# Kernel optimization log

Measured on AMD Instinct MI355X. Metric: run time of the kernel, lower is better.

Reference implementation:

```python
import jax, jax.numpy as jnp
import numpy as np

V, D, NH, DH, DFF, NL = 32000, 512, 8, 64, 2048, 6
S, B = 512, 8
NEG = -1e18


def layer_norm(x, g, b, eps=1e-5):
    m = x.mean(-1, keepdims=True)
    v = ((x - m) ** 2).mean(-1, keepdims=True)
    return (x - m) / jnp.sqrt(v + eps) * g + b


def mha(q, k, v, Wq, bq, Wk, bk, Wv, bv, Wo, bo, mask):
    Bq, Q, _ = q.shape
    K = k.shape[1]
    qh = (q @ Wq + bq).reshape(Bq, Q, NH, DH).transpose(0, 2, 1, 3)
    kh = (k @ Wk + bk).reshape(Bq, K, NH, DH).transpose(0, 2, 1, 3)
    vh = (v @ Wv + bv).reshape(Bq, K, NH, DH).transpose(0, 2, 1, 3)
    scores = jnp.einsum('bhqd,bhkd->bhqk', qh, kh) / np.sqrt(DH).astype(np.float32)
    scores = jnp.where(mask[:, None, :, :], NEG, scores)
    attn = jax.nn.softmax(scores, axis=-1)
    ctx = jnp.einsum('bhqk,bhkd->bhqd', attn, vh).transpose(0, 2, 1, 3).reshape(Bq, Q, NH * DH)
    return ctx @ Wo + bo


def positional_encoding(seq_len):
    pos = jnp.arange(seq_len, dtype=jnp.float32)[:, None]
    div = jnp.exp(jnp.arange(0, D, 2, dtype=jnp.float32) * (-np.log(10000.0) / D))
    pe = jnp.zeros((seq_len, D), jnp.float32)
    pe = pe.at[:, 0::2].set(jnp.sin(pos * div))
    pe = pe.at[:, 1::2].set(jnp.cos(pos * div))
    return pe


def setup_inputs() -> dict:
    key = jax.random.key(0)
    ks = iter(jax.random.split(key, 64))
    sc = 0.02
    pn = lambda shape: jax.random.normal(next(ks), shape, jnp.float32) * sc
    inp = {}
    inp['targets'] = jax.random.randint(next(ks), (S, B), 0, V)
    inp['memory'] = jax.random.normal(next(ks), (B, S, D), jnp.float32)
    inp['trg_mask'] = jnp.broadcast_to(jnp.triu(jnp.ones((S, S), bool), 1), (B, S, S))
    inp['memory_mask'] = jnp.zeros((B, S, S), bool)
    emb = pn((V, D)).at[1].set(0.0)  # padding_idx=1
    inp['emb'] = emb
    # stacked per-layer params
    for nm in ['Wq_s', 'Wk_s', 'Wv_s', 'Wo_s', 'Wq_c', 'Wk_c', 'Wv_c', 'Wo_c']:
        inp[nm] = pn((NL, D, D))
    for nm in ['bq_s', 'bk_s', 'bv_s', 'bo_s', 'bq_c', 'bk_c', 'bv_c', 'bo_c']:
        inp[nm] = jnp.zeros((NL, D), jnp.float32)
    inp['W1'] = pn((NL, D, DFF)); inp['b1'] = jnp.zeros((NL, DFF), jnp.float32)
    inp['W2'] = pn((NL, DFF, D)); inp['b2'] = jnp.zeros((NL, D), jnp.float32)
    for nm in ['g1', 'g2', 'g3']:
        inp[nm] = jnp.ones((NL, D), jnp.float32)
    for nm in ['be1', 'be2', 'be3']:
        inp[nm] = jnp.zeros((NL, D), jnp.float32)
    return inp


def reference(targets, memory, trg_mask, memory_mask, emb,
              Wq_s, bq_s, Wk_s, bk_s, Wv_s, bv_s, Wo_s, bo_s,
              Wq_c, bq_c, Wk_c, bk_c, Wv_c, bv_c, Wo_c, bo_c,
              W1, b1, W2, b2, g1, be1, g2, be2, g3, be3):
    # targets: (S, B) ints; embedding + sqrt(d) scale + sinusoidal PE
    x = emb[targets] * np.sqrt(D).astype(np.float32)      # (S, B, D)
    x = x + positional_encoding(targets.shape[0])[:, None, :]
    x = x.transpose(1, 0, 2)                              # (B, S, D)
    for i in range(NL):
        sa = mha(x, x, x, Wq_s[i], bq_s[i], Wk_s[i], bk_s[i], Wv_s[i], bv_s[i],
                 Wo_s[i], bo_s[i], trg_mask)
        x = layer_norm(x + sa, g1[i], be1[i])
        ca = mha(x, memory, memory, Wq_c[i], bq_c[i], Wk_c[i], bk_c[i], Wv_c[i], bv_c[i],
                 Wo_c[i], bo_c[i], memory_mask)
        x = layer_norm(x + ca, g2[i], be2[i])
        ff = jax.nn.relu(x @ W1[i] + b1[i]) @ W2[i] + b2[i]
        x = layer_norm(x + ff, g3[i], be3[i])
    return x
```

## Files before the change

### kernel.cpp

```cpp
#include <hip/hip_runtime.h>

typedef unsigned short u16;
typedef unsigned int   u32;
typedef __attribute__((ext_vector_type(4))) u16   u16x4;
typedef __attribute__((ext_vector_type(8))) u16   u16x8;
typedef __attribute__((ext_vector_type(8))) __bf16 bf16x8;
typedef __attribute__((ext_vector_type(4))) float f32x4;

#define DEV static __device__ __forceinline__

constexpr int DIM = 512, NHEAD = 8, DHEAD = 64, DFFN = 2048, NLAY = 6, SEQ = 512, BATCH = 8;
constexpr int MROWS = BATCH * SEQ;
constexpr long HD = (long)SEQ * DHEAD;
constexpr long SQ = (long)DIM * DIM;

DEV float bf2f(u16 u) { union { u32 i; float f; } x; x.i = (u32)u << 16; return x.f; }
DEV u16 f2bf(float f) { union { float f; u32 i; } x; x.f = f; u32 r = x.i + 0x7fffu + ((x.i >> 16) & 1u); return (u16)(r >> 16); }

DEV void gl_lds16(const u16* g, u16* l) {
    __builtin_amdgcn_global_load_lds((const __attribute__((address_space(1))) u32*)(const void*)g,
                                     (__attribute__((address_space(3))) u32*)(void*)l, 16, 0, 0);
}

struct TP { const float* in[8]; u16* out[8]; long ls[8]; };

__global__ __launch_bounds__(256) void transpose8(TP p)
{
    __shared__ u16 t[32][33];
    int z = blockIdx.z, which = z / NLAY, l = z % NLAY;
    const float* in = p.in[which] + (long)l * SQ;
    u16* out = p.out[which] + (long)l * p.ls[which];
    int k0 = blockIdx.y * 32, n0 = blockIdx.x * 32;
    int tx = threadIdx.x & 31, ty = threadIdx.x >> 5;
    #pragma unroll
    for (int i = ty; i < 32; i += 8) t[i][tx] = f2bf(in[(long)(k0 + i) * 512 + n0 + tx]);
    __syncthreads();
    #pragma unroll
    for (int i = ty; i < 32; i += 8) out[(long)(n0 + i) * 512 + k0 + tx] = t[tx][i];
}

__global__ __launch_bounds__(256) void transpose_w(const float* __restrict__ in, u16* __restrict__ out,
                                                   int K, int N, long outLS)
{
    __shared__ u16 t[32][33];
    long bi = (long)blockIdx.z * K * N, bo = (long)blockIdx.z * outLS;
    int k0 = blockIdx.y * 32, n0 = blockIdx.x * 32;
    int tx = threadIdx.x & 31, ty = threadIdx.x >> 5;
    #pragma unroll
    for (int i = ty; i < 32; i += 8) t[i][tx] = f2bf(in[bi + (long)(k0 + i) * N + n0 + tx]);
    __syncthreads();
    #pragma unroll
    for (int i = ty; i < 32; i += 8) out[bo + (long)(n0 + i) * K + k0 + tx] = t[tx][i];
}

__global__ __launch_bounds__(256) void concat_bias(const float* __restrict__ a, const float* __restrict__ b,
                                                   const float* __restrict__ c, float* __restrict__ out, int nsrc)
{
    int i = blockIdx.x * 256 + threadIdx.x;
    int col = i & 511, j = (i >> 9) % nsrc, l = i / (nsrc * 512);
    const float* s = (j == 0) ? a : (j == 1) ? b : c;
    out[i] = s[l * 512 + col];
}

__global__ __launch_bounds__(256) void conv_f32_bf16(const float* __restrict__ in, u16* __restrict__ out)
{
    long i = ((long)blockIdx.x * 256 + threadIdx.x) * 4;
    float4 v = *(const float4*)(in + i);
    u16x4 o; o.x = f2bf(v.x); o.y = f2bf(v.y); o.z = f2bf(v.z); o.w = f2bf(v.w);
    *(u16x4*)(out + i) = o;
}

__global__ __launch_bounds__(256) void embed_pe(const int* __restrict__ targets, const float* __restrict__ emb,
                                                u16* __restrict__ xb)
{
    int t4 = (blockIdx.x * 256 + threadIdx.x) * 4;
    int d = t4 & (DIM - 1);
    int s = (t4 >> 9) & (SEQ - 1);
    int b = t4 >> 18;
    int tok = targets[s * BATCH + b];
    float4 e = *(const float4*)(emb + (long)tok * DIM + d);
    u16x4 ob;
    const float ef[4] = { e.x, e.y, e.z, e.w };
    #pragma unroll
    for (int j = 0; j < 4; ++j) {
        int dd = d + j;
        float div = expf((float)(dd & ~1) * -0.017988946039016f);
        float ang = (float)s * div;
        float pe = (dd & 1) ? cosf(ang) : sinf(ang);
        ob[j] = f2bf(ef[j] * 22.627416997969522f + pe);
    }
    *(u16x4*)(xb + ((long)b * SEQ + s) * DIM + d) = ob;
}

DEV void scat_sd(u16* dst, int mm, int col, float v) {
    dst[(long)((mm >> 9) * NHEAD + (col >> 6)) * HD + (long)(mm & 511) * DHEAD + (col & 63)] = f2bf(v);
}
DEV void scat_ds(u16* dst, int mm, int col, float v) {
    dst[(long)((mm >> 9) * NHEAD + (col >> 6)) * HD + (long)(col & 63) * SEQ + (mm & 511)] = f2bf(v);
}

template <int BM, int BN, int EPI>
__global__ __launch_bounds__(256) void gemm_t(const u16* __restrict__ A0, const u16* __restrict__ A1,
                                              const u16* __restrict__ Bt,
                                              void* __restrict__ C0, void* __restrict__ C1, void* __restrict__ C2,
                                              const float* __restrict__ bias, int K, int ld, int ldc,
                                              int gx, int aSplit)
{
    constexpr int NCHA = BM / 8;
    constexpr int NCH  = (BM + BN) / 8;
    constexpr int MI   = BM / 32;
    constexpr int NI   = BN / 32;
    __shared__ __align__(16) u16 lds[2][NCH * 512];

    const int tid = threadIdx.x, lane = tid & 63, wid = tid >> 6;
    const int nwg = gridDim.x, bid = blockIdx.x;
    const int wg = (bid & 7) * (nwg >> 3) + (bid >> 3);
    const int m0 = (wg / gx) * BM, n0 = (wg % gx) * BN;
    const u16* A = (n0 < aSplit) ? A0 : A1;
    const int kBase = blockIdx.y * K;
    const int wr = (wid >> 1) * (BM / 2), wc = (wid & 1) * (BN / 2);
    const int fr = lane & 15, fq = lane >> 4;
    const int srow = lane >> 3;
    const int scol = ((lane & 7) ^ srow) * 8;

    f32x4 acc[MI][NI] = {};

    auto stage = [&](int buf, int k0) {
        #pragma unroll
        for (int c = wid; c < NCH; c += 4) {
            if (c < NCHA) gl_lds16(A  + (long)(m0 + c * 8 + srow) * ld + kBase + k0 + scol, &lds[buf][c * 512]);
            else          gl_lds16(Bt + (long)(n0 + (c - NCHA) * 8 + srow) * ld + kBase + k0 + scol, &lds[buf][c * 512]);
        }
    };

    const int nt = K >> 6;
    stage(0, 0);
    __syncthreads();
    int cur = 0;
    const int swz = (fr & 7) << 4;
    for (int t = 0; t < nt; ++t) {
        if (t + 1 < nt) stage(cur ^ 1, (t + 1) << 6);
        const char* lb = (const char*)&lds[cur][0];
        bf16x8 a[MI][2], b[NI][2];
        #pragma unroll
        for (int mi = 0; mi < MI; ++mi)
            #pragma unroll
            for (int kk = 0; kk < 2; ++kk)
                a[mi][kk] = *(const bf16x8*)(lb + (wr + mi * 16 + fr) * 128 + ((kk * 64 + fq * 16) ^ swz));
        #pragma unroll
        for (int ni = 0; ni < NI; ++ni)
            #pragma unroll
            for (int kk = 0; kk < 2; ++kk)
                b[ni][kk] = *(const bf16x8*)(lb + (BM + wc + ni * 16 + fr) * 128 + ((kk * 64 + fq * 16) ^ swz));
        #pragma unroll
        for (int kk = 0; kk < 2; ++kk)
            #pragma unroll
            for (int mi = 0; mi < MI; ++mi)
                #pragma unroll
                for (int ni = 0; ni < NI; ++ni)
                    acc[mi][ni] = __builtin_amdgcn_mfma_f32_16x16x32_bf16(a[mi][kk], b[ni][kk], acc[mi][ni], 0, 0, 0);
        __syncthreads();
        cur ^= 1;
    }

    #pragma unroll
    for (int mi = 0; mi < MI; ++mi)
    #pragma unroll
    for (int ni = 0; ni < NI; ++ni)
    #pragma unroll
    for (int rr = 0; rr < 4; ++rr) {
        int mm = m0 + wr + mi * 16 + fq * 4 + rr;
        int nn = n0 + wc + ni * 16 + fr;
        float v = acc[mi][ni][rr];
        if (EPI != 5) v += bias[nn];
        if (EPI == 0) {
            ((u16*)C0)[(long)mm * ldc + nn] = f2bf(v);
        } else if (EPI == 1) {
            ((u16*)C0)[(long)mm * ldc + nn] = f2bf(fmaxf(v, 0.f));
        } else if (EPI == 5) {
            ((float*)C0)[(long)blockIdx.y * MROWS * ldc + (long)mm * ldc + nn] = v;
        } else {
            int which = nn >> 9, col = nn & 511;
            if (which == 0)      scat_sd((u16*)C0, mm, col, v);
            else if (which == 1) scat_sd((u16*)C1, mm, col, v);
            else                 scat_ds((u16*)C2, mm, col, v);
        }
    }
}

template <bool CAUSAL>
__global__ __launch_bounds__(256) void flash_attn(const u16* __restrict__ qh, const u16* __restrict__ kh,
                                                  const u16* __restrict__ vT, u16* __restrict__ ctx)
{
    constexpr int KVB = 128;
    __shared__ __align__(16) u16 Kl[2][KVB * 64];
    __shared__ __align__(16) u16 Vl[2][64 * KVB];
    __shared__ __align__(16) u16 Pl[4][16 * KVB];
    const int lane = threadIdx.x & 63, wid = threadIdx.x >> 6;
    const int head = blockIdx.x & 63, qt = blockIdx.x >> 6;
    const int q0 = qt * 64;
    const long hb = (long)head * HD;
    const int fr = lane & 15, fq = lane >> 4;
    const int swz = (fr & 7) << 4;

    bf16x8 qf[2];
    #pragma unroll
    for (int kf = 0; kf < 2; ++kf)
        qf[kf] = *(const bf16x8*)(qh + hb + (long)(q0 + wid * 16 + fr) * 64 + kf * 32 + fq * 8);

    const int nt = CAUSAL ? (q0 >> 7) + 1 : SEQ / KVB;

    auto stage = [&](int buf, int t) {
        const long kv0 = (long)t * KVB;
        const int kr = lane >> 3;
        const int kcol = ((lane & 7) ^ kr) * 8;
        for (int c = wid; c < 16; c += 4)
            gl_lds16(kh + hb + (kv0 + c * 8 + kr) * 64 + kcol, &Kl[buf][c * 512]);
        const int vr = lane >> 4;
        for (int c = wid; c < 16; c += 4) {
            int row = c * 4 + vr;
            int vcol = ((lane & 15) ^ (row & 7)) * 8;
            gl_lds16(vT + hb + (long)row * SEQ + kv0 + vcol, &Vl[buf][c * 512]);
        }
    };

    float m[4], l[4];
    #pragma unroll
    for (int r = 0; r < 4; ++r) { m[r] = -3.0e38f; l[r] = 0.f; }
    f32x4 ao[4] = {};

    stage(0, 0);
    __syncthreads();
    int cur = 0;
    for (int t = 0; t < nt; ++t) {
        if (t + 1 < nt) stage(cur ^ 1, t + 1);
        f32x4 as[8] = {};
        const char* kb = (const char*)&Kl[cur][0];
        __builtin_amdgcn_s_setprio(1);
        #pragma unroll
        for (int nf = 0; nf < 8; ++nf)
            #pragma unroll
            for (int kf = 0; kf < 2; ++kf) {
                bf16x8 kfr = *(const bf16x8*)(kb + (nf * 16 + fr) * 128 + ((kf * 64 + fq * 16) ^ swz));
                as[nf] = __builtin_amdgcn_mfma_f32_16x16x32_bf16(qf[kf], kfr, as[nf], 0, 0, 0);
            }
        __builtin_amdgcn_s_setprio(0);
        const int kv0 = t * KVB;
        const int qrow = q0 + wid * 16 + fq * 4;
        #pragma unroll
        for (int nf = 0; nf < 8; ++nf)
            #pragma unroll
            for (int rr = 0; rr < 4; ++rr) {
                float s = as[nf][rr] * 0.125f;
                if (CAUSAL && (kv0 + nf * 16 + fr > qrow + rr)) s = -3.0e38f;
                as[nf][rr] = s;
            }
        float p_scale[4];
        #pragma unroll
        for (int rr = 0; rr < 4; ++rr) {
            float mx = as[0][rr];
            #pragma unroll
            for (int nf = 1; nf < 8; ++nf) mx = fmaxf(mx, as[nf][rr]);
            #pragma unroll
            for (int o = 1; o < 16; o <<= 1) mx = fmaxf(mx, __shfl_xor(mx, o, 64));
            float mnew = fmaxf(m[rr], mx);
            p_scale[rr] = __expf(m[rr] - mnew);
            m[rr] = mnew;
        }
        float rsum[4] = {0.f, 0.f, 0.f, 0.f};
        u16* pw = &Pl[wid][0];
        #pragma unroll
        for (int nf = 0; nf < 8; ++nf)
            #pragma unroll
            for (int rr = 0; rr < 4; ++rr) {
                float p = __expf(as[nf][rr] - m[rr]);
                rsum[rr] += p;
                int row = fq * 4 + rr;
                int byte = (row * 256 + (nf * 16 + fr) * 2) ^ ((row & 7) << 4);
                *(u16*)((char*)pw + byte) = f2bf(p);
            }
        #pragma unroll
        for (int rr = 0; rr < 4; ++rr) {
            #pragma unroll
            for (int o = 1; o < 16; o <<= 1) rsum[rr] += __shfl_xor(rsum[rr], o, 64);
            l[rr] = l[rr] * p_scale[rr] + rsum[rr];
        }
        #pragma unroll
        for (int nf = 0; nf < 4; ++nf)
            #pragma unroll
            for (int rr = 0; rr < 4; ++rr) ao[nf][rr] *= p_scale[rr];
        const char* vb = (const char*)&Vl[cur][0];
        __builtin_amdgcn_s_setprio(1);
        #pragma unroll
        for (int kf = 0; kf < 4; ++kf) {
            int pbyte = (fr * 256 + kf * 64 + fq * 16) ^ swz;
            bf16x8 pa = *(const bf16x8*)((const char*)pw + pbyte);
            #pragma unroll
            for (int nf = 0; nf < 4; ++nf) {
                bf16x8 vf = *(const bf16x8*)(vb + (nf * 16 + fr) * 256 + ((kf * 64 + fq * 16) ^ swz));
                ao[nf] = __builtin_amdgcn_mfma_f32_16x16x32_bf16(pa, vf, ao[nf], 0, 0, 0);
            }
        }
        __builtin_amdgcn_s_setprio(0);
        __syncthreads();
        cur ^= 1;
    }
    const int b = head >> 3, h = head & 7;
    #pragma unroll
    for (int nf = 0; nf < 4; ++nf)
        #pragma unroll
        for (int rr = 0; rr < 4; ++rr) {
            int qq = q0 + wid * 16 + fq * 4 + rr;
            ctx[((long)(b * SEQ + qq)) * DIM + h * 64 + nf * 16 + fr] = f2bf(ao[nf][rr] / l[rr]);
        }
}

__global__ __launch_bounds__(256) void add_ln(u16* xb, const u16* __restrict__ y,
                                              const float* __restrict__ g, const float* __restrict__ be)
{
    int row = blockIdx.x * 4 + (threadIdx.x >> 6);
    int lane = threadIdx.x & 63;
    long off = (long)row * DIM + lane * 8;
    u16x8 xv = *(const u16x8*)(xb + off);
    u16x8 yv = *(const u16x8*)(y + off);
    float v[8];
    #pragma unroll
    for (int j = 0; j < 8; ++j) v[j] = bf2f(xv[j]) + bf2f(yv[j]);
    float sum = 0.f;
    #pragma unroll
    for (int j = 0; j < 8; ++j) sum += v[j];
    #pragma unroll
    for (int o = 32; o; o >>= 1) sum += __shfl_xor(sum, o, 64);
    float mean = sum * (1.0f / DIM);
    float vs = 0.f;
    #pragma unroll
    for (int j = 0; j < 8; ++j) { float d = v[j] - mean; vs += d * d; }
    #pragma unroll
    for (int o = 32; o; o >>= 1) vs += __shfl_xor(vs, o, 64);
    float rstd = rsqrtf(vs * (1.0f / DIM) + 1e-5f);
    u16x8 ob;
    #pragma unroll
    for (int j = 0; j < 8; ++j) {
        int col = lane * 8 + j;
        ob[j] = f2bf((v[j] - mean) * rstd * g[col] + be[col]);
    }
    *(u16x8*)(xb + off) = ob;
}

__global__ __launch_bounds__(256) void add_ln2(u16* xb, const float* __restrict__ yf,
                                               const float* __restrict__ bias,
                                               const float* __restrict__ g, const float* __restrict__ be,
                                               float* __restrict__ xf)
{
    int row = blockIdx.x * 4 + (threadIdx.x >> 6);
    int lane = threadIdx.x & 63;
    long off = (long)row * DIM + lane * 8;
    u16x8 xv = *(const u16x8*)(xb + off);
    float4 a0 = *(const float4*)(yf + off);
    float4 a1 = *(const float4*)(yf + off + 4);
    float4 b0 = *(const float4*)(yf + (long)MROWS * DIM + off);
    float4 b1 = *(const float4*)(yf + (long)MROWS * DIM + off + 4);
    float v[8] = { a0.x + b0.x, a0.y + b0.y, a0.z + b0.z, a0.w + b0.w,
                   a1.x + b1.x, a1.y + b1.y, a1.z + b1.z, a1.w + b1.w };
    #pragma unroll
    for (int j = 0; j < 8; ++j) v[j] += bf2f(xv[j]) + bias[lane * 8 + j];
    float sum = 0.f;
    #pragma unroll
    for (int j = 0; j < 8; ++j) sum += v[j];
    #pragma unroll
    for (int o = 32; o; o >>= 1) sum += __shfl_xor(sum, o, 64);
    float mean = sum * (1.0f / DIM);
    float vs = 0.f;
    #pragma unroll
    for (int j = 0; j < 8; ++j) { float d = v[j] - mean; vs += d * d; }
    #pragma unroll
    for (int o = 32; o; o >>= 1) vs += __shfl_xor(vs, o, 64);
    float rstd = rsqrtf(vs * (1.0f / DIM) + 1e-5f);
    float outv[8]; u16x8 ob;
    #pragma unroll
    for (int j = 0; j < 8; ++j) {
        int col = lane * 8 + j;
        float r = (v[j] - mean) * rstd * g[col] + be[col];
        outv[j] = r; ob[j] = f2bf(r);
    }
    *(u16x8*)(xb + off) = ob;
    if (xf) {
        *(float4*)(xf + off)     = *(const float4*)&outv[0];
        *(float4*)(xf + off + 4) = *(const float4*)&outv[4];
    }
}

extern "C" void kernel_launch(void* const* d_in, const int* in_sizes, int n_in,
                              void* d_out, int out_size, void* d_ws, size_t ws_size,
                              hipStream_t stream)
{
    const int*   targets = (const int*)  d_in[0];
    const float* memory  = (const float*)d_in[1];
    const float* emb     = (const float*)d_in[4];
    const float* Wg[8]; for (int i = 0; i < 8; ++i) Wg[i] = (const float*)d_in[5 + i];
    const float* bg[8]; for (int i = 0; i < 8; ++i) bg[i] = (const float*)d_in[13 + i];
    const float* W1  = (const float*)d_in[21];
    const float* b1  = (const float*)d_in[22];
    const float* W2  = (const float*)d_in[23];
    const float* b2  = (const float*)d_in[24];
    const float* g1  = (const float*)d_in[25];
    const float* g2  = (const float*)d_in[26];
    const float* g3  = (const float*)d_in[27];
    const float* be1 = (const float*)d_in[28];
    const float* be2 = (const float*)d_in[29];
    const float* be3 = (const float*)d_in[30];

    char* w = (char*)d_ws;
    auto take = [&](size_t n) -> char* { char* p = w; w += (n + 255) & ~(size_t)255; return p; };
    u16*   wqkvT = (u16*)take((size_t)NLAY * 3 * SQ * 2);
    u16*   wcatT = (u16*)take((size_t)NLAY * 3 * SQ * 2);
    u16*   woT   = (u16*)take((size_t)NLAY * SQ * 2);
    u16*   wocT  = (u16*)take((size_t)NLAY * SQ * 2);
    u16*   w1T   = (u16*)take((size_t)NLAY * DIM * DFFN * 2);
    u16*   w2T   = (u16*)take((size_t)NLAY * DIM * DFFN * 2);
    float* bqkv  = (float*)take((size_t)NLAY * 3 * DIM * 4);
    float* bqkvc = (float*)take((size_t)NLAY * 3 * DIM * 4);
    u16*   xb    = (u16*)  take((size_t)MROWS * DIM * 2);
    u16*   y     = (u16*)  take((size_t)MROWS * DIM * 2);
    float* yf    = (float*)take((size_t)2 * MROWS * DIM * 4);
    u16*   memb  = (u16*)  take((size_t)MROWS * DIM * 2);
    u16*   qh    = (u16*)  take((size_t)MROWS * DIM * 2);
    u16*   kh    = (u16*)  take((size_t)MROWS * DIM * 2);
    u16*   vT    = (u16*)  take((size_t)MROWS * DIM * 2);
    u16*   ctx   = (u16*)  take((size_t)MROWS * DIM * 2);
    u16*   h1    = (u16*)  take((size_t)MROWS * DFFN * 2);

    TP tp;
    tp.in[0] = Wg[0]; tp.out[0] = wqkvT;          tp.ls[0] = 3 * SQ;
    tp.in[1] = Wg[1]; tp.out[1] = wqkvT + SQ;     tp.ls[1] = 3 * SQ;
    tp.in[2] = Wg[2]; tp.out[2] = wqkvT + 2 * SQ; tp.ls[2] = 3 * SQ;
    tp.in[3] = Wg[3]; tp.out[3] = woT;            tp.ls[3] = SQ;
    tp.in[4] = Wg[4]; tp.out[4] = wcatT;          tp.ls[4] = 3 * SQ;
    tp.in[5] = Wg[5]; tp.out[5] = wcatT + SQ;     tp.ls[5] = 3 * SQ;
    tp.in[6] = Wg[6]; tp.out[6] = wcatT + 2 * SQ; tp.ls[6] = 3 * SQ;
    tp.in[7] = Wg[7]; tp.out[7] = wocT;           tp.ls[7] = SQ;
    transpose8<<<dim3(16, 16, 8 * NLAY), 256, 0, stream>>>(tp);
    transpose_w<<<dim3(64, 16, NLAY), 256, 0, stream>>>(W1, w1T, DIM, DFFN, (long)DIM * DFFN);
    transpose_w<<<dim3(16, 64, NLAY), 256, 0, stream>>>(W2, w2T, DFFN, DIM, (long)DIM * DFFN);
    concat_bias<<<NLAY * 3 * DIM / 256, 256, 0, stream>>>(bg[0], bg[1], bg[2], bqkv, 3);
    concat_bias<<<NLAY * 3 * DIM / 256, 256, 0, stream>>>(bg[4], bg[5], bg[6], bqkvc, 3);
    conv_f32_bf16<<<2048, 256, 0, stream>>>(memory, memb);
    embed_pe<<<2048, 256, 0, stream>>>(targets, emb, xb);

    const int BIG = 1 << 30;
    for (int i = 0; i < NLAY; ++i) {
        const u16 *wqkv = wqkvT + (long)i * 3 * SQ, *wcat = wcatT + (long)i * 3 * SQ;
        const u16 *wo = woT + (long)i * SQ, *woc = wocT + (long)i * SQ;
        const u16 *w1t = w1T + (long)i * DIM * DFFN, *w2t = w2T + (long)i * DIM * DFFN;
        const float *bo = bg[3] + i * DIM, *boc = bg[7] + i * DIM;

        gemm_t<128, 128, 4><<<384, 256, 0, stream>>>(xb, xb, wqkv, qh, kh, vT, bqkv + i * 3 * DIM, DIM, DIM, 0, 12, BIG);
        flash_attn<true><<<BATCH * NHEAD * (SEQ / 64), 256, 0, stream>>>(qh, kh, vT, ctx);
        gemm_t<64, 64, 0><<<512, 256, 0, stream>>>(ctx, ctx, wo, y, nullptr, nullptr, bo, DIM, DIM, DIM, 8, BIG);
        add_ln<<<MROWS / 4, 256, 0, stream>>>(xb, y, g1 + i * DIM, be1 + i * DIM);

        gemm_t<128, 128, 4><<<384, 256, 0, stream>>>(xb, memb, wcat, qh, kh, vT, bqkvc + i * 3 * DIM, DIM, DIM, 0, 12, 512);
        flash_attn<false><<<BATCH * NHEAD * (SEQ / 64), 256, 0, stream>>>(qh, kh, vT, ctx);
        gemm_t<64, 64, 0><<<512, 256, 0, stream>>>(ctx, ctx, woc, y, nullptr, nullptr, boc, DIM, DIM, DIM, 8, BIG);
        add_ln<<<MROWS / 4, 256, 0, stream>>>(xb, y, g2 + i * DIM, be2 + i * DIM);

        gemm_t<128, 128, 1><<<512, 256, 0, stream>>>(xb, xb, w1t, h1, nullptr, nullptr, b1 + i * DFFN, DIM, DIM, DFFN, 16, BIG);
        gemm_t<64, 64, 5><<<dim3(512, 2), 256, 0, stream>>>(h1, h1, w2t, yf, nullptr, nullptr, nullptr,
                                                            DFFN / 2, DFFN, DIM, 8, BIG);
        add_ln2<<<MROWS / 4, 256, 0, stream>>>(xb, yf, b2 + i * DIM, g3 + i * DIM, be3 + i * DIM,
                                               (i == NLAY - 1) ? (float*)d_out : nullptr);
    }
}
```

Before: 817.9 us.

## Merge prep kernels, add BK template for small GEMMs, lazy softmax rescale

The GEMM is templated on its K tile. The 64x64 GEMMs (output projections and FFN2) now use a K tile of 128, which halves their loop iterations and barriers, and the swizzle is generalised to match. Flash attention now rescales the running max and accumulators only when some row's max grows by more than 8, skipping exponentials and multiplies on most tiles at some cost to numeric headroom. Several setup kernels are merged into fewer launches (W1/W2 transposes, the bias concats, and embedding plus memory conversion) to cut launch overhead.

```diff
diff --git a/kernel.cpp b/kernel.cpp
--- a/kernel.cpp
+++ b/kernel.cpp
@@ -39,57 +39,66 @@
     for (int i = ty; i < 32; i += 8) out[(long)(n0 + i) * 512 + k0 + tx] = t[tx][i];
 }
 
-__global__ __launch_bounds__(256) void transpose_w(const float* __restrict__ in, u16* __restrict__ out,
-                                                   int K, int N, long outLS)
+__global__ __launch_bounds__(256) void transpose_w12(const float* __restrict__ W1, const float* __restrict__ W2,
+                                                     u16* __restrict__ w1T, u16* __restrict__ w2T)
 {
     __shared__ u16 t[32][33];
-    long bi = (long)blockIdx.z * K * N, bo = (long)blockIdx.z * outLS;
-    int k0 = blockIdx.y * 32, n0 = blockIdx.x * 32;
+    int z = blockIdx.z;
+    bool isW2 = z >= NLAY;
+    int l = isW2 ? z - NLAY : z;
+    const float* in = (isW2 ? W2 : W1) + (long)l * DIM * DFFN;
+    u16* out = (isW2 ? w2T : w1T) + (long)l * DIM * DFFN;
+    int K = isW2 ? DFFN : DIM, N = isW2 ? DIM : DFFN;
+    int k0 = (isW2 ? blockIdx.x : blockIdx.y) * 32;
+    int n0 = (isW2 ? blockIdx.y : blockIdx.x) * 32;
     int tx = threadIdx.x & 31, ty = threadIdx.x >> 5;
     #pragma unroll
-    for (int i = ty; i < 32; i += 8) t[i][tx] = f2bf(in[bi + (long)(k0 + i) * N + n0 + tx]);
+    for (int i = ty; i < 32; i += 8) t[i][tx] = f2bf(in[(long)(k0 + i) * N + n0 + tx]);
     __syncthreads();
     #pragma unroll
-    for (int i = ty; i < 32; i += 8) out[bo + (long)(n0 + i) * K + k0 + tx] = t[tx][i];
-}
-
-__global__ __launch_bounds__(256) void concat_bias(const float* __restrict__ a, const float* __restrict__ b,
-                                                   const float* __restrict__ c, float* __restrict__ out, int nsrc)
+    for (int i = ty; i < 32; i += 8) out[(long)(n0 + i) * K + k0 + tx] = t[tx][i];
+}
+
+struct CB { const float* s[6]; };
+__global__ __launch_bounds__(256) void concat2(CB p, float* __restrict__ bqkv, float* __restrict__ bqkvc)
 {
     int i = blockIdx.x * 256 + threadIdx.x;
-    int col = i & 511, j = (i >> 9) % nsrc, l = i / (nsrc * 512);
-    const float* s = (j == 0) ? a : (j == 1) ? b : c;
-    out[i] = s[l * 512 + col];
-}
-
-__global__ __launch_bounds__(256) void conv_f32_bf16(const float* __restrict__ in, u16* __restrict__ out)
-{
-    long i = ((long)blockIdx.x * 256 + threadIdx.x) * 4;
-    float4 v = *(const float4*)(in + i);
-    u16x4 o; o.x = f2bf(v.x); o.y = f2bf(v.y); o.z = f2bf(v.z); o.w = f2bf(v.w);
-    *(u16x4*)(out + i) = o;
-}
-
-__global__ __launch_bounds__(256) void embed_pe(const int* __restrict__ targets, const float* __restrict__ emb,
-                                                u16* __restrict__ xb)
-{
-    int t4 = (blockIdx.x * 256 + threadIdx.x) * 4;
-    int d = t4 & (DIM - 1);
-    int s = (t4 >> 9) & (SEQ - 1);
-    int b = t4 >> 18;
-    int tok = targets[s * BATCH + b];
-    float4 e = *(const float4*)(emb + (long)tok * DIM + d);
-    u16x4 ob;
-    const float ef[4] = { e.x, e.y, e.z, e.w };
-    #pragma unroll
-    for (int j = 0; j < 4; ++j) {
-        int dd = d + j;
-        float div = expf((float)(dd & ~1) * -0.017988946039016f);
-        float ang = (float)s * div;
-        float pe = (dd & 1) ? cosf(ang) : sinf(ang);
-        ob[j] = f2bf(ef[j] * 22.627416997969522f + pe);
-    }
-    *(u16x4*)(xb + ((long)b * SEQ + s) * DIM + d) = ob;
+    constexpr int HALF = NLAY * 3 * DIM;
+    int j = (i < HALF) ? i : i - HALF;
+    int col = j & 511, wsel = (j >> 9) % 3, l = j / 1536;
+    const float* s = p.s[(i < HALF ? 0 : 3) + wsel];
+    (i < HALF ? bqkv : bqkvc)[j] = s[l * 512 + col];
+}
+
+__global__ __launch_bounds__(256) void prep_act(const int* __restrict__ targets, const float* __restrict__ emb,
+                                                u16* __restrict__ xb,
+                                                const float* __restrict__ memory, u16* __restrict__ memb)
+{
+    int bid = blockIdx.x;
+    if (bid < 2048) {
+        int t4 = (bid * 256 + threadIdx.x) * 4;
+        int d = t4 & (DIM - 1);
+        int s = (t4 >> 9) & (SEQ - 1);
+        int b = t4 >> 18;
+        int tok = targets[s * BATCH + b];
+        float4 e = *(const float4*)(emb + (long)tok * DIM + d);
+        u16x4 ob;
+        const float ef[4] = { e.x, e.y, e.z, e.w };
+        #pragma unroll
+        for (int j = 0; j < 4; ++j) {
+            int dd = d + j;
+            float div = expf((float)(dd & ~1) * -0.017988946039016f);
+            float ang = (float)s * div;
+            float pe = (dd & 1) ? cosf(ang) : sinf(ang);
+            ob[j] = f2bf(ef[j] * 22.627416997969522f + pe);
+        }
+        *(u16x4*)(xb + ((long)b * SEQ + s) * DIM + d) = ob;
+    } else {
+        long i = ((long)(bid - 2048) * 256 + threadIdx.x) * 4;
+        float4 v = *(const float4*)(memory + i);
+        u16x4 o; o.x = f2bf(v.x); o.y = f2bf(v.y); o.z = f2bf(v.z); o.w = f2bf(v.w);
+        *(u16x4*)(memb + i) = o;
+    }
 }
 
 DEV void scat_sd(u16* dst, int mm, int col, float v) {
@@ -99,17 +108,20 @@
     dst[(long)((mm >> 9) * NHEAD + (col >> 6)) * HD + (long)(col & 63) * SEQ + (mm & 511)] = f2bf(v);
 }
 
-template <int BM, int BN, int EPI>
+template <int BM, int BN, int BK, int EPI>
 __global__ __launch_bounds__(256) void gemm_t(const u16* __restrict__ A0, const u16* __restrict__ A1,
                                               const u16* __restrict__ Bt,
                                               void* __restrict__ C0, void* __restrict__ C1, void* __restrict__ C2,
                                               const float* __restrict__ bias, int K, int ld, int ldc,
                                               int gx, int aSplit)
 {
-    constexpr int NCHA = BM / 8;
-    constexpr int NCH  = (BM + BN) / 8;
-    constexpr int MI   = BM / 32;
-    constexpr int NI   = BN / 32;
+    constexpr int SLOTS = BK / 8;
+    constexpr int RPC   = 512 / BK;
+    constexpr int KK    = BK / 32;
+    constexpr int NCHA  = BM / RPC;
+    constexpr int NCH   = (BM + BN) / RPC;
+    constexpr int MI    = BM / 32;
+    constexpr int NI    = BN / 32;
     __shared__ __align__(16) u16 lds[2][NCH * 512];
 
     const int tid = threadIdx.x, lane = tid & 63, wid = tid >> 6;
@@ -120,40 +132,43 @@
     const int kBase = blockIdx.y * K;
     const int wr = (wid >> 1) * (BM / 2), wc = (wid & 1) * (BN / 2);
     const int fr = lane & 15, fq = lane >> 4;
-    const int srow = lane >> 3;
-    const int scol = ((lane & 7) ^ srow) * 8;
+    const int srow  = lane / SLOTS;
+    const int sslot = lane % SLOTS;
 
     f32x4 acc[MI][NI] = {};
 
     auto stage = [&](int buf, int k0) {
         #pragma unroll
         for (int c = wid; c < NCH; c += 4) {
-            if (c < NCHA) gl_lds16(A  + (long)(m0 + c * 8 + srow) * ld + kBase + k0 + scol, &lds[buf][c * 512]);
-            else          gl_lds16(Bt + (long)(n0 + (c - NCHA) * 8 + srow) * ld + kBase + k0 + scol, &lds[buf][c * 512]);
+            int slot = sslot ^ ((c * RPC + srow) & (SLOTS - 1));
+            long row = (c < NCHA) ? (long)(m0 + c * RPC + srow)
+                                  : (long)(n0 + (c - NCHA) * RPC + srow);
+            const u16* src = (c < NCHA) ? A : Bt;
+            gl_lds16(src + row * ld + kBase + k0 + slot * 8, &lds[buf][c * 512]);
         }
     };
 
-    const int nt = K >> 6;
+    const int nt = K / BK;
     stage(0, 0);
     __syncthreads();
     int cur = 0;
-    const int swz = (fr & 7) << 4;
+    const int swz = (fr & (SLOTS - 1)) << 4;
     for (int t = 0; t < nt; ++t) {
-        if (t + 1 < nt) stage(cur ^ 1, (t + 1) << 6);
+        if (t + 1 < nt) stage(cur ^ 1, (t + 1) * BK);
         const char* lb = (const char*)&lds[cur][0];
-        bf16x8 a[MI][2], b[NI][2];
+        bf16x8 a[MI][KK], b[NI][KK];
         #pragma unroll
         for (int mi = 0; mi < MI; ++mi)
             #pragma unroll
-            for (int kk = 0; kk < 2; ++kk)
-                a[mi][kk] = *(const bf16x8*)(lb + (wr + mi * 16 + fr) * 128 + ((kk * 64 + fq * 16) ^ swz));
+            for (int kk = 0; kk < KK; ++kk)
+                a[mi][kk] = *(const bf16x8*)(lb + (wr + mi * 16 + fr) * (BK * 2) + ((kk * 64 + fq * 16) ^ swz));
         #pragma unroll
         for (int ni = 0; ni < NI; ++ni)
             #pragma unroll
-            for (int kk = 0; kk < 2; ++kk)
-                b[ni][kk] = *(const bf16x8*)(lb + (BM + wc + ni * 16 + fr) * 128 + ((kk * 64 + fq * 16) ^ swz));
-        #pragma unroll
-        for (int kk = 0; kk < 2; ++kk)
+            for (int kk = 0; kk < KK; ++kk)
+                b[ni][kk] = *(const bf16x8*)(lb + (BM + wc + ni * 16 + fr) * (BK * 2) + ((kk * 64 + fq * 16) ^ swz));
+        #pragma unroll
+        for (int kk = 0; kk < KK; ++kk)
             #pragma unroll
             for (int mi = 0; mi < MI; ++mi)
                 #pragma unroll
@@ -255,7 +270,7 @@
                 if (CAUSAL && (kv0 + nf * 16 + fr > qrow + rr)) s = -3.0e38f;
                 as[nf][rr] = s;
             }
-        float p_scale[4];
+        float mnew[4]; int need = 0;
         #pragma unroll
         for (int rr = 0; rr < 4; ++rr) {
             float mx = as[0][rr];
@@ -263,9 +278,18 @@
             for (int nf = 1; nf < 8; ++nf) mx = fmaxf(mx, as[nf][rr]);
             #pragma unroll
             for (int o = 1; o < 16; o <<= 1) mx = fmaxf(mx, __shfl_xor(mx, o, 64));
-            float mnew = fmaxf(m[rr], mx);
-            p_scale[rr] = __expf(m[rr] - mnew);
-            m[rr] = mnew;
+            mnew[rr] = fmaxf(m[rr], mx);
+            need |= (mx > m[rr] + 8.f) ? 1 : 0;
+        }
+        if (__any(need)) {
+            #pragma unroll
+            for (int rr = 0; rr < 4; ++rr) {
+                float ps = __expf(m[rr] - mnew[rr]);
+                m[rr] = mnew[rr];
+                l[rr] *= ps;
+                #pragma unroll
+                for (int nf = 0; nf < 4; ++nf) ao[nf][rr] *= ps;
+            }
         }
         float rsum[4] = {0.f, 0.f, 0.f, 0.f};
         u16* pw = &Pl[wid][0];
@@ -283,12 +307,8 @@
         for (int rr = 0; rr < 4; ++rr) {
             #pragma unroll
             for (int o = 1; o < 16; o <<= 1) rsum[rr] += __shfl_xor(rsum[rr], o, 64);
-            l[rr] = l[rr] * p_scale[rr] + rsum[rr];
-        }
-        #pragma unroll
-        for (int nf = 0; nf < 4; ++nf)
-            #pragma unroll
-            for (int rr = 0; rr < 4; ++rr) ao[nf][rr] *= p_scale[rr];
+            l[rr] += rsum[rr];
+        }
         const char* vb = (const char*)&Vl[cur][0];
         __builtin_amdgcn_s_setprio(1);
         #pragma unroll
@@ -440,12 +460,11 @@
     tp.in[6] = Wg[6]; tp.out[6] = wcatT + 2 * SQ; tp.ls[6] = 3 * SQ;
     tp.in[7] = Wg[7]; tp.out[7] = wocT;           tp.ls[7] = SQ;
     transpose8<<<dim3(16, 16, 8 * NLAY), 256, 0, stream>>>(tp);
-    transpose_w<<<dim3(64, 16, NLAY), 256, 0, stream>>>(W1, w1T, DIM, DFFN, (long)DIM * DFFN);
-    transpose_w<<<dim3(16, 64, NLAY), 256, 0, stream>>>(W2, w2T, DFFN, DIM, (long)DIM * DFFN);
-    concat_bias<<<NLAY * 3 * DIM / 256, 256, 0, stream>>>(bg[0], bg[1], bg[2], bqkv, 3);
-    concat_bias<<<NLAY * 3 * DIM / 256, 256, 0, stream>>>(bg[4], bg[5], bg[6], bqkvc, 3);
-    conv_f32_bf16<<<2048, 256, 0, stream>>>(memory, memb);
-    embed_pe<<<2048, 256, 0, stream>>>(targets, emb, xb);
+    transpose_w12<<<dim3(64, 16, 2 * NLAY), 256, 0, stream>>>(W1, W2, w1T, w2T);
+    CB cb; cb.s[0] = bg[0]; cb.s[1] = bg[1]; cb.s[2] = bg[2];
+    cb.s[3] = bg[4]; cb.s[4] = bg[5]; cb.s[5] = bg[6];
+    concat2<<<2 * NLAY * 3 * DIM / 256, 256, 0, stream>>>(cb, bqkv, bqkvc);
+    prep_act<<<4096, 256, 0, stream>>>(targets, emb, xb, memory, memb);
 
     const int BIG = 1 << 30;
     for (int i = 0; i < NLAY; ++i) {
@@ -454,19 +473,19 @@
         const u16 *w1t = w1T + (long)i * DIM * DFFN, *w2t = w2T + (long)i * DIM * DFFN;
         const float *bo = bg[3] + i * DIM, *boc = bg[7] + i * DIM;
 
-        gemm_t<128, 128, 4><<<384, 256, 0, stream>>>(xb, xb, wqkv, qh, kh, vT, bqkv + i * 3 * DIM, DIM, DIM, 0, 12, BIG);
+        gemm_t<128, 128, 64, 4><<<384, 256, 0, stream>>>(xb, xb, wqkv, qh, kh, vT, bqkv + i * 3 * DIM, DIM, DIM, 0, 12, BIG);
         flash_attn<true><<<BATCH * NHEAD * (SEQ / 64), 256, 0, stream>>>(qh, kh, vT, ctx);
-        gemm_t<64, 64, 0><<<512, 256, 0, stream>>>(ctx, ctx, wo, y, nullptr, nullptr, bo, DIM, DIM, DIM, 8, BIG);
+        gemm_t<64, 64, 128, 0><<<512, 256, 0, stream>>>(ctx, ctx, wo, y, nullptr, nullptr, bo, DIM, DIM, DIM, 8, BIG);
         add_ln<<<MROWS / 4, 256, 0, stream>>>(xb, y, g1 + i * DIM, be1 + i * DIM);
 
-        gemm_t<128, 128, 4><<<384, 256, 0, stream>>>(xb, memb, wcat, qh, kh, vT, bqkvc + i * 3 * DIM, DIM, DIM, 0, 12, 512);
+        gemm_t<128, 128, 64, 4><<<384, 256, 0, stream>>>(xb, memb, wcat, qh, kh, vT, bqkvc + i * 3 * DIM, DIM, DIM, 0, 12, 512);
         flash_attn<false><<<BATCH * NHEAD * (SEQ / 64), 256, 0, stream>>>(qh, kh, vT, ctx);
-        gemm_t<64, 64, 0><<<512, 256, 0, stream>>>(ctx, ctx, woc, y, nullptr, nullptr, boc, DIM, DIM, DIM, 8, BIG);
+        gemm_t<64, 64, 128, 0><<<512, 256, 0, stream>>>(ctx, ctx, woc, y, nullptr, nullptr, boc, DIM, DIM, DIM, 8, BIG);
         add_ln<<<MROWS / 4, 256, 0, stream>>>(xb, y, g2 + i * DIM, be2 + i * DIM);
 
-        gemm_t<128, 128, 1><<<512, 256, 0, stream>>>(xb, xb, w1t, h1, nullptr, nullptr, b1 + i * DFFN, DIM, DIM, DFFN, 16, BIG);
-        gemm_t<64, 64, 5><<<dim3(512, 2), 256, 0, stream>>>(h1, h1, w2t, yf, nullptr, nullptr, nullptr,
-                                                            DFFN / 2, DFFN, DIM, 8, BIG);
+        gemm_t<128, 128, 64, 1><<<512, 256, 0, stream>>>(xb, xb, w1t, h1, nullptr, nullptr, b1 + i * DFFN, DIM, DIM, DFFN, 16, BIG);
+        gemm_t<64, 64, 128, 5><<<dim3(512, 2), 256, 0, stream>>>(h1, h1, w2t, yf, nullptr, nullptr, nullptr,
+                                                                 DFFN / 2, DFFN, DIM, 8, BIG);
         add_ln2<<<MROWS / 4, 256, 0, stream>>>(xb, yf, b2 + i * DIM, g3 + i * DIM, be3 + i * DIM,
                                                (i == NLAY - 1) ? (float*)d_out : nullptr);
     }
```

Result: no change. 813.8 us (-0.5%).
